# Optimization experiments

Hardware: AMD Instinct MI355X
Metric: run time of the kernel (lower is better)

The kernel has to match this reference:

```python
import jax, jax.numpy as jnp
import numpy as np

N_NODES = 50000
N_EDGES = 800000
IN_DIM = 128
OUT_DIM = 64
NEG_SLOPE = 0.01  # torch F.leaky_relu default


def setup_inputs() -> dict:
    key = jax.random.key(0)
    k1, k2, k3, k4, k5 = jax.random.split(key, 5)
    features = jax.random.normal(k1, (N_NODES, IN_DIM), dtype=jnp.float32)
    # xavier-ish scale for weights
    fc_w = jax.random.normal(k2, (OUT_DIM, IN_DIM), dtype=jnp.float32) * (1.0 / np.sqrt(IN_DIM))
    attn_w = jax.random.normal(k3, (2 * OUT_DIM,), dtype=jnp.float32) * (1.0 / np.sqrt(2 * OUT_DIM))
    src = jax.random.randint(k4, (N_EDGES,), 0, N_NODES, dtype=jnp.int32)
    dst = jax.random.randint(k5, (N_EDGES,), 0, N_NODES, dtype=jnp.int32)
    return {"features": features, "fc_w": fc_w, "attn_w": attn_w, "src": src, "dst": dst}


def reference(features, fc_w, attn_w, src, dst):
    n = features.shape[0]
    out_dim = fc_w.shape[0]
    # z = fc(features), [N, out_dim]
    z = features @ fc_w.T
    # attn_fc([z_src || z_dst]) = z_src @ w_src + z_dst @ w_dst
    a_src = z @ attn_w[:out_dim]   # [N]
    a_dst = z @ attn_w[out_dim:]   # [N]
    e = a_src[src] + a_dst[dst]    # [E] per-edge raw score
    e = jnp.where(e > 0, e, NEG_SLOPE * e)  # leaky_relu
    # edge softmax over incoming edges of each dst node
    e_max = jax.ops.segment_max(e, dst, num_segments=n)      # [N]
    w = jnp.exp(e - e_max[dst])                               # [E]
    denom = jax.ops.segment_sum(w, dst, num_segments=n)       # [N]
    # weighted neighbor sum: sum_e alpha_e * z[src_e]
    num = jax.ops.segment_sum(w[:, None] * z[src], dst, num_segments=n)  # [N, out_dim]
    h = num / jnp.where(denom > 0, denom, 1.0)[:, None]
    # activation = elu
    h = jax.nn.elu(h)
    return h
```

## Files before the change

kernel.cpp:

```cpp
#include <hip/hip_runtime.h>
#include <hip/hip_bf16.h>
#include <hip/hip_fp16.h>

#define N_NODES 50000
#define N_EDGES 800000
#define IN_DIM 128
#define OUT_DIM 64
#define NEG_SLOPE 0.01f
#define NEG_INF (-3.0e38f)

#define N_STRIPS (N_NODES / 16)
#define Z_BLOCKS ((N_STRIPS + 3) / 4)
#define E_I4 (N_EDGES / 4)

#define NB ((N_NODES + 127) / 128)
#define CAP_B 3072
#define CNT_STRIDE 16
#define EB 100
#define CHUNK_I4 (E_I4 / EB)

typedef __bf16 bf16x8 __attribute__((ext_vector_type(8)));
typedef float f32x4 __attribute__((ext_vector_type(4)));

__device__ __forceinline__ unsigned short f2bf_us(float f) {
  __hip_bfloat16 h = __float2bfloat16(f);
  return *reinterpret_cast<unsigned short*>(&h);
}
__device__ __forceinline__ bf16x8 pack_bf16(float4 lo, float4 hi) {
  union { bf16x8 v; unsigned short u[8]; } r;
  r.u[0] = f2bf_us(lo.x); r.u[1] = f2bf_us(lo.y);
  r.u[2] = f2bf_us(lo.z); r.u[3] = f2bf_us(lo.w);
  r.u[4] = f2bf_us(hi.x); r.u[5] = f2bf_us(hi.y);
  r.u[6] = f2bf_us(hi.z); r.u[7] = f2bf_us(hi.w);
  return r.v;
}
__device__ __forceinline__ float bflo(unsigned u) {
  return __uint_as_float(u << 16);
}
__device__ __forceinline__ float bfhi(unsigned u) {
  return __uint_as_float(u & 0xffff0000u);
}

__global__ __launch_bounds__(256) void gat_z_bucket(
    const float* __restrict__ feat, const float* __restrict__ fcw,
    const float* __restrict__ attnw, __hip_bfloat16* __restrict__ z,
    float* __restrict__ asrc, float* __restrict__ adst,
    const int* __restrict__ src, const int* __restrict__ dst,
    int* __restrict__ cnt, unsigned* __restrict__ pairs) {
  if (blockIdx.x >= Z_BLOCKS) {
    __shared__ int hist[NB];
    __shared__ int curs[NB];
    const int tid = threadIdx.x;
    const int i0 = (blockIdx.x - Z_BLOCKS) * CHUNK_I4;
    for (int i = tid; i < NB; i += 256) hist[i] = 0;
    __syncthreads();
    for (int t = i0 + tid; t < i0 + CHUNK_I4; t += 256) {
      int4 d = ((const int4*)dst)[t];
      atomicAdd(&hist[d.x >> 7], 1);
      atomicAdd(&hist[d.y >> 7], 1);
      atomicAdd(&hist[d.z >> 7], 1);
      atomicAdd(&hist[d.w >> 7], 1);
    }
    __syncthreads();
    for (int i = tid; i < NB; i += 256) {
      int h = hist[i];
      curs[i] = h ? atomicAdd(cnt + i * CNT_STRIDE, h) : 0;
    }
    __syncthreads();
    for (int t = i0 + tid; t < i0 + CHUNK_I4; t += 256) {
      int4 s = ((const int4*)src)[t];
      int4 d = ((const int4*)dst)[t];
#define BKT_PUT(dd, ss)                                                    \
  {                                                                        \
    int b = (dd) >> 7;                                                     \
    int r = atomicAdd(&curs[b], 1);                                        \
    if (r < CAP_B)                                                         \
      pairs[(size_t)b * CAP_B + r] =                                       \
          ((unsigned)((dd) & 127) << 16) | (unsigned)(ss);                 \
  }
      BKT_PUT(d.x, s.x)
      BKT_PUT(d.y, s.y)
      BKT_PUT(d.z, s.z)
      BKT_PUT(d.w, s.w)
#undef BKT_PUT
    }
    return;
  }

  const int lane = threadIdx.x & 63;
  const int m = lane & 15;
  const int quad = lane >> 4;
  const int wv = blockIdx.x * 4 + (threadIdx.x >> 6);
  if (wv >= N_STRIPS) return;
  const int n0 = wv * 16;

  bf16x8 bfrag[4][4];
#pragma unroll
  for (int t = 0; t < 4; ++t) {
    const float* wr = fcw + (size_t)(m + 16 * t) * IN_DIM + quad * 8;
#pragma unroll
    for (int c = 0; c < 4; ++c) {
      float4 lo = *(const float4*)(wr + c * 32);
      float4 hi = *(const float4*)(wr + c * 32 + 4);
      bfrag[t][c] = pack_bf16(lo, hi);
    }
  }

  f32x4 acc[4] = {{0.f, 0.f, 0.f, 0.f}, {0.f, 0.f, 0.f, 0.f},
                  {0.f, 0.f, 0.f, 0.f}, {0.f, 0.f, 0.f, 0.f}};
  const float* ar = feat + (size_t)(n0 + m) * IN_DIM + quad * 8;
#pragma unroll
  for (int c = 0; c < 4; ++c) {
    float4 lo = *(const float4*)(ar + c * 32);
    float4 hi = *(const float4*)(ar + c * 32 + 4);
    const bf16x8 af = pack_bf16(lo, hi);
#pragma unroll
    for (int t = 0; t < 4; ++t)
      acc[t] = __builtin_amdgcn_mfma_f32_16x16x32_bf16(af, bfrag[t][c],
                                                       acc[t], 0, 0, 0);
  }

#pragma unroll
  for (int t = 0; t < 4; ++t)
#pragma unroll
    for (int r = 0; r < 4; ++r)
      z[(size_t)(n0 + quad * 4 + r) * OUT_DIM + m + 16 * t] =
          __float2bfloat16(acc[t][r]);

  float aws[4], awd[4];
#pragma unroll
  for (int t = 0; t < 4; ++t) {
    aws[t] = attnw[m + 16 * t];
    awd[t] = attnw[OUT_DIM + m + 16 * t];
  }
  float ps[4], pd[4];
#pragma unroll
  for (int r = 0; r < 4; ++r) {
    float s = 0.f, d = 0.f;
#pragma unroll
    for (int t = 0; t < 4; ++t) {
      s = fmaf(acc[t][r], aws[t], s);
      d = fmaf(acc[t][r], awd[t], d);
    }
    ps[r] = s;
    pd[r] = d;
  }
#pragma unroll
  for (int off = 1; off < 16; off <<= 1) {
#pragma unroll
    for (int r = 0; r < 4; ++r) {
      ps[r] += __shfl_xor(ps[r], off, 64);
      pd[r] += __shfl_xor(pd[r], off, 64);
    }
  }
  if (m == 0) {
#pragma unroll
    for (int r = 0; r < 4; ++r) {
      asrc[n0 + quad * 4 + r] = ps[r];
      adst[n0 + quad * 4 + r] = pd[r];
    }
  }
}

__global__ __launch_bounds__(256) void gat_build_csr(
    const unsigned* __restrict__ pairs, const int* __restrict__ cnt,
    int* __restrict__ offsets, int* __restrict__ ssorted) {
  __shared__ int hist[128], exo[128], cur[128], wsum[4];
  const int b = blockIdx.x;
  const int tid = threadIdx.x;

  int ls = 0;
  for (int i = tid; i < b; i += 256) ls += cnt[i * CNT_STRIDE];
#pragma unroll
  for (int off = 32; off; off >>= 1) ls += __shfl_xor(ls, off, 64);
  if ((tid & 63) == 0) wsum[tid >> 6] = ls;
  if (tid < 128) hist[tid] = 0;
  __syncthreads();
  const int base = wsum[0] + wsum[1] + wsum[2] + wsum[3];

  const int c = min(cnt[b * CNT_STRIDE], CAP_B);
  const unsigned* bp = pairs + (size_t)b * CAP_B;
  for (int i = tid; i < c; i += 256) atomicAdd(&hist[bp[i] >> 16], 1);
  __syncthreads();

  if (tid < 128) exo[tid] = hist[tid];
  __syncthreads();
  for (int off = 1; off < 128; off <<= 1) {
    int u = (tid >= off && tid < 128) ? exo[tid - off] : 0;
    __syncthreads();
    if (tid < 128) exo[tid] += u;
    __syncthreads();
  }
  if (tid < 128) {
    const int ex = exo[tid] - hist[tid];
    cur[tid] = ex;
    const int node = b * 128 + tid;
    if (node < N_NODES) offsets[node] = base + ex;
  }
  if (b == NB - 1 && tid == 0) offsets[N_NODES] = base + c;
  __syncthreads();

  for (int i = tid; i < c; i += 256) {
    const unsigned p = bp[i];
    const int r = atomicAdd(&cur[p >> 16], 1);
    ssorted[base + r] = (int)(p & 0xFFFFu);
  }
}

__global__ __launch_bounds__(256) void gat_agg(
    const __hip_bfloat16* __restrict__ zb, const float* __restrict__ asrc,
    const float* __restrict__ adst, const int* __restrict__ offsets,
    const int* __restrict__ ssorted, float* __restrict__ out) {
  const int lane = threadIdx.x & 63;
  const int j = lane & 7;
  const int eg = lane >> 3;
  const int node = (blockIdx.x * blockDim.x + threadIdx.x) >> 6;
  if (node >= N_NODES) return;
  const uint4* __restrict__ zp4 = (const uint4*)zb;
  const int o0 = offsets[node];
  const int o1 = offsets[node + 1];
  float4* __restrict__ orow = (float4*)(out + (size_t)node * OUT_DIM);
  if (o0 == o1) {
    if (eg == 0) {
      const float4 zv = {0.f, 0.f, 0.f, 0.f};
      orow[2 * j] = zv;
      orow[2 * j + 1] = zv;
    }
    return;
  }
  const float ad = adst[node];

  float m = NEG_INF, dsum = 0.f;
  float acca[8] = {0.f, 0.f, 0.f, 0.f, 0.f, 0.f, 0.f, 0.f};
  float accb[8] = {0.f, 0.f, 0.f, 0.f, 0.f, 0.f, 0.f, 0.f};

  for (int base = o0; base < o1; base += 64) {
    const int cnt = min(64, o1 - base);
    int s = 0;
    float ev = NEG_INF;
    if (lane < cnt) {
      s = ssorted[base + lane];
      float v = asrc[s] + ad;
      ev = v > 0.f ? v : NEG_SLOPE * v;
    }
    float cm = ev;
#pragma unroll
    for (int off = 32; off; off >>= 1) cm = fmaxf(cm, __shfl_xor(cm, off, 64));
    const float nm = fmaxf(m, cm);
    const float scale = __expf(m - nm);
    dsum *= scale;
#pragma unroll
    for (int c = 0; c < 8; ++c) {
      acca[c] *= scale;
      accb[c] *= scale;
    }
    m = nm;

    const float w = (lane < cnt) ? __expf(ev - m) : 0.f;
    dsum += w;
    const unsigned pk =
        (unsigned)s |
        ((unsigned)__half_as_ushort(__float2half(w)) << 16);

    const int ngr = (cnt + 7) >> 3;
    for (int g = 0; g < ngr; g += 2) {
      const unsigned pa = __shfl(pk, 8 * g + eg, 64);
      const int sa = (int)(pa & 0xFFFFu);
      const float wa = __half2float(__ushort_as_half((unsigned short)(pa >> 16)));
      const uint4 ua = zp4[(size_t)sa * 8 + j];
      if (g + 1 < ngr) {
        const unsigned pb = __shfl(pk, 8 * (g + 1) + eg, 64);
        const int sb = (int)(pb & 0xFFFFu);
        const float wb =
            __half2float(__ushort_as_half((unsigned short)(pb >> 16)));
        const uint4 ub = zp4[(size_t)sb * 8 + j];
        accb[0] = fmaf(wb, bflo(ub.x), accb[0]);
        accb[1] = fmaf(wb, bfhi(ub.x), accb[1]);
        accb[2] = fmaf(wb, bflo(ub.y), accb[2]);
        accb[3] = fmaf(wb, bfhi(ub.y), accb[3]);
        accb[4] = fmaf(wb, bflo(ub.z), accb[4]);
        accb[5] = fmaf(wb, bfhi(ub.z), accb[5]);
        accb[6] = fmaf(wb, bflo(ub.w), accb[6]);
        accb[7] = fmaf(wb, bfhi(ub.w), accb[7]);
      }
      acca[0] = fmaf(wa, bflo(ua.x), acca[0]);
      acca[1] = fmaf(wa, bfhi(ua.x), acca[1]);
      acca[2] = fmaf(wa, bflo(ua.y), acca[2]);
      acca[3] = fmaf(wa, bfhi(ua.y), acca[3]);
      acca[4] = fmaf(wa, bflo(ua.z), acca[4]);
      acca[5] = fmaf(wa, bfhi(ua.z), acca[5]);
      acca[6] = fmaf(wa, bflo(ua.w), acca[6]);
      acca[7] = fmaf(wa, bfhi(ua.w), acca[7]);
    }
  }

  float acc[8];
#pragma unroll
  for (int c = 0; c < 8; ++c) acc[c] = acca[c] + accb[c];
#pragma unroll
  for (int off = 8; off < 64; off <<= 1)
#pragma unroll
    for (int c = 0; c < 8; ++c) acc[c] += __shfl_xor(acc[c], off, 64);
#pragma unroll
  for (int off = 32; off; off >>= 1) dsum += __shfl_xor(dsum, off, 64);

  if (eg == 0) {
    const float inv = 1.f / (dsum > 0.f ? dsum : 1.f);
    float4 r0, r1;
    float h;
    h = acc[0] * inv; r0.x = h > 0.f ? h : expm1f(h);
    h = acc[1] * inv; r0.y = h > 0.f ? h : expm1f(h);
    h = acc[2] * inv; r0.z = h > 0.f ? h : expm1f(h);
    h = acc[3] * inv; r0.w = h > 0.f ? h : expm1f(h);
    h = acc[4] * inv; r1.x = h > 0.f ? h : expm1f(h);
    h = acc[5] * inv; r1.y = h > 0.f ? h : expm1f(h);
    h = acc[6] * inv; r1.z = h > 0.f ? h : expm1f(h);
    h = acc[7] * inv; r1.w = h > 0.f ? h : expm1f(h);
    orow[2 * j] = r0;
    orow[2 * j + 1] = r1;
  }
}

extern "C" void kernel_launch(void* const* d_in, const int* in_sizes, int n_in,
                              void* d_out, int out_size, void* d_ws, size_t ws_size,
                              hipStream_t stream) {
  const float* feat  = (const float*)d_in[0];
  const float* fcw   = (const float*)d_in[1];
  const float* attnw = (const float*)d_in[2];
  const int* src     = (const int*)d_in[3];
  const int* dst     = (const int*)d_in[4];
  float* out = (float*)d_out;

  char* ws = (char*)d_ws;
  __hip_bfloat16* z = (__hip_bfloat16*)ws;
  ws += (size_t)N_NODES * OUT_DIM * sizeof(__hip_bfloat16);
  float* asrc = (float*)ws;   ws += (size_t)N_NODES * sizeof(float);
  float* adst = (float*)ws;   ws += (size_t)N_NODES * sizeof(float);
  int* cnt = (int*)ws;        ws += (size_t)NB * CNT_STRIDE * sizeof(int);
  int* offsets = (int*)ws;    ws += (size_t)(N_NODES + 4) * sizeof(int);
  unsigned* pairs = (unsigned*)ws; ws += (size_t)NB * CAP_B * sizeof(unsigned);
  int* ssorted = (int*)ws;    ws += (size_t)N_EDGES * sizeof(int);

  hipMemsetAsync(cnt, 0, (size_t)NB * CNT_STRIDE * sizeof(int), stream);

  gat_z_bucket<<<Z_BLOCKS + EB, 256, 0, stream>>>(
      feat, fcw, attnw, z, asrc, adst, src, dst, cnt, pairs);
  gat_build_csr<<<NB, 256, 0, stream>>>(pairs, cnt, offsets, ssorted);
  gat_agg<<<(N_NODES * 64 + 255) / 256, 256, 0, stream>>>(z, asrc, adst,
                                                          offsets, ssorted, out);
}
```

Measured before the change: 145.3 us.

## Fuse per-bucket CSR build into aggregation kernel using shared-memory sorted sources

Merges the CSR-building and aggregation kernels into one. Each 512-thread block takes half of a 128-node bucket, histograms and scans its 64 nodes in shared memory, scatters source indices into LDS, then runs the online-softmax aggregation with each wave handling 8 nodes. This removes one launch, the global offsets/ssorted writes and their re-reads. In exchange each bucket's pairs are read twice (once per half) and there are fewer, larger blocks with 12KB of LDS each, which can leave load imbalance across waves.

```diff
diff --git a/kernel.cpp b/kernel.cpp
--- a/kernel.cpp
+++ b/kernel.cpp
@@ -162,162 +162,165 @@
   }
 }
 
-__global__ __launch_bounds__(256) void gat_build_csr(
+__global__ __launch_bounds__(512) void gat_csr_agg(
     const unsigned* __restrict__ pairs, const int* __restrict__ cnt,
-    int* __restrict__ offsets, int* __restrict__ ssorted) {
-  __shared__ int hist[128], exo[128], cur[128], wsum[4];
-  const int b = blockIdx.x;
+    const __hip_bfloat16* __restrict__ zb, const float* __restrict__ asrc,
+    const float* __restrict__ adst, float* __restrict__ out) {
+  __shared__ int hist[64];
+  __shared__ int noff[65];
+  __shared__ int cur[64];
+  __shared__ int lsrc[CAP_B];
   const int tid = threadIdx.x;
-
-  int ls = 0;
-  for (int i = tid; i < b; i += 256) ls += cnt[i * CNT_STRIDE];
-#pragma unroll
-  for (int off = 32; off; off >>= 1) ls += __shfl_xor(ls, off, 64);
-  if ((tid & 63) == 0) wsum[tid >> 6] = ls;
-  if (tid < 128) hist[tid] = 0;
+  const int b = blockIdx.x >> 1;
+  const int half = blockIdx.x & 1;
+  const int c = min(cnt[b * CNT_STRIDE], CAP_B);
+  const unsigned* __restrict__ bp = pairs + (size_t)b * CAP_B;
+
+  if (tid < 64) hist[tid] = 0;
   __syncthreads();
-  const int base = wsum[0] + wsum[1] + wsum[2] + wsum[3];
-
-  const int c = min(cnt[b * CNT_STRIDE], CAP_B);
-  const unsigned* bp = pairs + (size_t)b * CAP_B;
-  for (int i = tid; i < c; i += 256) atomicAdd(&hist[bp[i] >> 16], 1);
+  for (int i = tid; i < c; i += 512) {
+    const int ln = (int)(bp[i] >> 16);
+    if ((ln >> 6) == half) atomicAdd(&hist[ln & 63], 1);
+  }
   __syncthreads();
-
-  if (tid < 128) exo[tid] = hist[tid];
+  if (tid < 64) {
+    const int h = hist[tid];
+    int s = h;
+#pragma unroll
+    for (int off = 1; off < 64; off <<= 1) {
+      const int u = __shfl_up(s, off, 64);
+      if (tid >= off) s += u;
+    }
+    noff[tid] = s - h;
+    cur[tid] = s - h;
+    if (tid == 63) noff[64] = s;
+  }
   __syncthreads();
-  for (int off = 1; off < 128; off <<= 1) {
-    int u = (tid >= off && tid < 128) ? exo[tid - off] : 0;
-    __syncthreads();
-    if (tid < 128) exo[tid] += u;
-    __syncthreads();
-  }
-  if (tid < 128) {
-    const int ex = exo[tid] - hist[tid];
-    cur[tid] = ex;
-    const int node = b * 128 + tid;
-    if (node < N_NODES) offsets[node] = base + ex;
-  }
-  if (b == NB - 1 && tid == 0) offsets[N_NODES] = base + c;
+  for (int i = tid; i < c; i += 512) {
+    const unsigned p = bp[i];
+    const int ln = (int)(p >> 16);
+    if ((ln >> 6) == half) {
+      const int r = atomicAdd(&cur[ln & 63], 1);
+      lsrc[r] = (int)(p & 0xFFFFu);
+    }
+  }
   __syncthreads();
 
-  for (int i = tid; i < c; i += 256) {
-    const unsigned p = bp[i];
-    const int r = atomicAdd(&cur[p >> 16], 1);
-    ssorted[base + r] = (int)(p & 0xFFFFu);
-  }
-}
-
-__global__ __launch_bounds__(256) void gat_agg(
-    const __hip_bfloat16* __restrict__ zb, const float* __restrict__ asrc,
-    const float* __restrict__ adst, const int* __restrict__ offsets,
-    const int* __restrict__ ssorted, float* __restrict__ out) {
-  const int lane = threadIdx.x & 63;
+  const int lane = tid & 63;
+  const int wv = tid >> 6;
   const int j = lane & 7;
   const int eg = lane >> 3;
-  const int node = (blockIdx.x * blockDim.x + threadIdx.x) >> 6;
-  if (node >= N_NODES) return;
   const uint4* __restrict__ zp4 = (const uint4*)zb;
-  const int o0 = offsets[node];
-  const int o1 = offsets[node + 1];
-  float4* __restrict__ orow = (float4*)(out + (size_t)node * OUT_DIM);
-  if (o0 == o1) {
+
+#pragma unroll 1
+  for (int k = 0; k < 8; ++k) {
+    const int ln = wv * 8 + k;
+    const int node = b * 128 + half * 64 + ln;
+    if (node >= N_NODES) break;
+    const int o0 = noff[ln];
+    const int o1 = noff[ln + 1];
+    float4* __restrict__ orow = (float4*)(out + (size_t)node * OUT_DIM);
+    if (o0 == o1) {
+      if (eg == 0) {
+        const float4 zv = {0.f, 0.f, 0.f, 0.f};
+        orow[2 * j] = zv;
+        orow[2 * j + 1] = zv;
+      }
+      continue;
+    }
+    const float ad = adst[node];
+
+    float m = NEG_INF, dsum = 0.f;
+    float acca[8] = {0.f, 0.f, 0.f, 0.f, 0.f, 0.f, 0.f, 0.f};
+    float accb[8] = {0.f, 0.f, 0.f, 0.f, 0.f, 0.f, 0.f, 0.f};
+
+    for (int base = o0; base < o1; base += 64) {
+      const int cnt2 = min(64, o1 - base);
+      int s = 0;
+      float ev = NEG_INF;
+      if (lane < cnt2) {
+        s = lsrc[base + lane];
+        const float v = asrc[s] + ad;
+        ev = v > 0.f ? v : NEG_SLOPE * v;
+      }
+      float cm = ev;
+#pragma unroll
+      for (int off = 32; off; off >>= 1)
+        cm = fmaxf(cm, __shfl_xor(cm, off, 64));
+      const float nm = fmaxf(m, cm);
+      const float scale = __expf(m - nm);
+      dsum *= scale;
+#pragma unroll
+      for (int cc = 0; cc < 8; ++cc) {
+        acca[cc] *= scale;
+        accb[cc] *= scale;
+      }
+      m = nm;
+
+      const float w = (lane < cnt2) ? __expf(ev - m) : 0.f;
+      dsum += w;
+      const unsigned pk =
+          (unsigned)s |
+          ((unsigned)__half_as_ushort(__float2half(w)) << 16);
+
+      const int ngr = (cnt2 + 7) >> 3;
+      for (int g = 0; g < ngr; g += 2) {
+        const unsigned pa = __shfl(pk, 8 * g + eg, 64);
+        const int sa = (int)(pa & 0xFFFFu);
+        const float wa =
+            __half2float(__ushort_as_half((unsigned short)(pa >> 16)));
+        const uint4 ua = zp4[(size_t)sa * 8 + j];
+        if (g + 1 < ngr) {
+          const unsigned pb = __shfl(pk, 8 * (g + 1) + eg, 64);
+          const int sb = (int)(pb & 0xFFFFu);
+          const float wb =
+              __half2float(__ushort_as_half((unsigned short)(pb >> 16)));
+          const uint4 ub = zp4[(size_t)sb * 8 + j];
+          accb[0] = fmaf(wb, bflo(ub.x), accb[0]);
+          accb[1] = fmaf(wb, bfhi(ub.x), accb[1]);
+          accb[2] = fmaf(wb, bflo(ub.y), accb[2]);
+          accb[3] = fmaf(wb, bfhi(ub.y), accb[3]);
+          accb[4] = fmaf(wb, bflo(ub.z), accb[4]);
+          accb[5] = fmaf(wb, bfhi(ub.z), accb[5]);
+          accb[6] = fmaf(wb, bflo(ub.w), accb[6]);
+          accb[7] = fmaf(wb, bfhi(ub.w), accb[7]);
+        }
+        acca[0] = fmaf(wa, bflo(ua.x), acca[0]);
+        acca[1] = fmaf(wa, bfhi(ua.x), acca[1]);
+        acca[2] = fmaf(wa, bflo(ua.y), acca[2]);
+        acca[3] = fmaf(wa, bfhi(ua.y), acca[3]);
+        acca[4] = fmaf(wa, bflo(ua.z), acca[4]);
+        acca[5] = fmaf(wa, bfhi(ua.z), acca[5]);
+        acca[6] = fmaf(wa, bflo(ua.w), acca[6]);
+        acca[7] = fmaf(wa, bfhi(ua.w), acca[7]);
+      }
+    }
+
+    float acc[8];
+#pragma unroll
+    for (int cc = 0; cc < 8; ++cc) acc[cc] = acca[cc] + accb[cc];
+#pragma unroll
+    for (int off = 8; off < 64; off <<= 1)
+#pragma unroll
+      for (int cc = 0; cc < 8; ++cc) acc[cc] += __shfl_xor(acc[cc], off, 64);
+#pragma unroll
+    for (int off = 32; off; off >>= 1) dsum += __shfl_xor(dsum, off, 64);
+
     if (eg == 0) {
-      const float4 zv = {0.f, 0.f, 0.f, 0.f};
-      orow[2 * j] = zv;
-      orow[2 * j + 1] = zv;
-    }
-    return;
-  }
-  const float ad = adst[node];
-
-  float m = NEG_INF, dsum = 0.f;
-  float acca[8] = {0.f, 0.f, 0.f, 0.f, 0.f, 0.f, 0.f, 0.f};
-  float accb[8] = {0.f, 0.f, 0.f, 0.f, 0.f, 0.f, 0.f, 0.f};
-
-  for (int base = o0; base < o1; base += 64) {
-    const int cnt = min(64, o1 - base);
-    int s = 0;
-    float ev = NEG_INF;
-    if (lane < cnt) {
-      s = ssorted[base + lane];
-      float v = asrc[s] + ad;
-      ev = v > 0.f ? v : NEG_SLOPE * v;
-    }
-    float cm = ev;
-#pragma unroll
-    for (int off = 32; off; off >>= 1) cm = fmaxf(cm, __shfl_xor(cm, off, 64));
-    const float nm = fmaxf(m, cm);
-    const float scale = __expf(m - nm);
-    dsum *= scale;
-#pragma unroll
-    for (int c = 0; c < 8; ++c) {
-      acca[c] *= scale;
-      accb[c] *= scale;
-    }
-    m = nm;
-
-    const float w = (lane < cnt) ? __expf(ev - m) : 0.f;
-    dsum += w;
-    const unsigned pk =
-        (unsigned)s |
-        ((unsigned)__half_as_ushort(__float2half(w)) << 16);
-
-    const int ngr = (cnt + 7) >> 3;
-    for (int g = 0; g < ngr; g += 2) {
-      const unsigned pa = __shfl(pk, 8 * g + eg, 64);
-      const int sa = (int)(pa & 0xFFFFu);
-      const float wa = __half2float(__ushort_as_half((unsigned short)(pa >> 16)));
-      const uint4 ua = zp4[(size_t)sa * 8 + j];
-      if (g + 1 < ngr) {
-        const unsigned pb = __shfl(pk, 8 * (g + 1) + eg, 64);
-        const int sb = (int)(pb & 0xFFFFu);
-        const float wb =
-            __half2float(__ushort_as_half((unsigned short)(pb >> 16)));
-        const uint4 ub = zp4[(size_t)sb * 8 + j];
-        accb[0] = fmaf(wb, bflo(ub.x), accb[0]);
-        accb[1] = fmaf(wb, bfhi(ub.x), accb[1]);
-        accb[2] = fmaf(wb, bflo(ub.y), accb[2]);
-        accb[3] = fmaf(wb, bfhi(ub.y), accb[3]);
-        accb[4] = fmaf(wb, bflo(ub.z), accb[4]);
-        accb[5] = fmaf(wb, bfhi(ub.z), accb[5]);
-        accb[6] = fmaf(wb, bflo(ub.w), accb[6]);
-        accb[7] = fmaf(wb, bfhi(ub.w), accb[7]);
-      }
-      acca[0] = fmaf(wa, bflo(ua.x), acca[0]);
-      acca[1] = fmaf(wa, bfhi(ua.x), acca[1]);
-      acca[2] = fmaf(wa, bflo(ua.y), acca[2]);
-      acca[3] = fmaf(wa, bfhi(ua.y), acca[3]);
-      acca[4] = fmaf(wa, bflo(ua.z), acca[4]);
-      acca[5] = fmaf(wa, bfhi(ua.z), acca[5]);
-      acca[6] = fmaf(wa, bflo(ua.w), acca[6]);
-      acca[7] = fmaf(wa, bfhi(ua.w), acca[7]);
-    }
-  }
-
-  float acc[8];
-#pragma unroll
-  for (int c = 0; c < 8; ++c) acc[c] = acca[c] + accb[c];
-#pragma unroll
-  for (int off = 8; off < 64; off <<= 1)
-#pragma unroll
-    for (int c = 0; c < 8; ++c) acc[c] += __shfl_xor(acc[c], off, 64);
-#pragma unroll
-  for (int off = 32; off; off >>= 1) dsum += __shfl_xor(dsum, off, 64);
-
-  if (eg == 0) {
-    const float inv = 1.f / (dsum > 0.f ? dsum : 1.f);
-    float4 r0, r1;
-    float h;
-    h = acc[0] * inv; r0.x = h > 0.f ? h : expm1f(h);
-    h = acc[1] * inv; r0.y = h > 0.f ? h : expm1f(h);
-    h = acc[2] * inv; r0.z = h > 0.f ? h : expm1f(h);
-    h = acc[3] * inv; r0.w = h > 0.f ? h : expm1f(h);
-    h = acc[4] * inv; r1.x = h > 0.f ? h : expm1f(h);
-    h = acc[5] * inv; r1.y = h > 0.f ? h : expm1f(h);
-    h = acc[6] * inv; r1.z = h > 0.f ? h : expm1f(h);
-    h = acc[7] * inv; r1.w = h > 0.f ? h : expm1f(h);
-    orow[2 * j] = r0;
-    orow[2 * j + 1] = r1;
+      const float inv = 1.f / (dsum > 0.f ? dsum : 1.f);
+      float4 r0, r1;
+      float h;
+      h = acc[0] * inv; r0.x = h > 0.f ? h : expm1f(h);
+      h = acc[1] * inv; r0.y = h > 0.f ? h : expm1f(h);
+      h = acc[2] * inv; r0.z = h > 0.f ? h : expm1f(h);
+      h = acc[3] * inv; r0.w = h > 0.f ? h : expm1f(h);
+      h = acc[4] * inv; r1.x = h > 0.f ? h : expm1f(h);
+      h = acc[5] * inv; r1.y = h > 0.f ? h : expm1f(h);
+      h = acc[6] * inv; r1.z = h > 0.f ? h : expm1f(h);
+      h = acc[7] * inv; r1.w = h > 0.f ? h : expm1f(h);
+      orow[2 * j] = r0;
+      orow[2 * j + 1] = r1;
+    }
   }
 }
 
@@ -337,15 +340,11 @@
   float* asrc = (float*)ws;   ws += (size_t)N_NODES * sizeof(float);
   float* adst = (float*)ws;   ws += (size_t)N_NODES * sizeof(float);
   int* cnt = (int*)ws;        ws += (size_t)NB * CNT_STRIDE * sizeof(int);
-  int* offsets = (int*)ws;    ws += (size_t)(N_NODES + 4) * sizeof(int);
   unsigned* pairs = (unsigned*)ws; ws += (size_t)NB * CAP_B * sizeof(unsigned);
-  int* ssorted = (int*)ws;    ws += (size_t)N_EDGES * sizeof(int);
 
   hipMemsetAsync(cnt, 0, (size_t)NB * CNT_STRIDE * sizeof(int), stream);
 
   gat_z_bucket<<<Z_BLOCKS + EB, 256, 0, stream>>>(
       feat, fcw, attnw, z, asrc, adst, src, dst, cnt, pairs);
-  gat_build_csr<<<NB, 256, 0, stream>>>(pairs, cnt, offsets, ssorted);
-  gat_agg<<<(N_NODES * 64 + 255) / 256, 256, 0, stream>>>(z, asrc, adst,
-                                                          offsets, ssorted, out);
-}
+  gat_csr_agg<<<NB * 2, 512, 0, stream>>>(pairs, cnt, z, asrc, adst, out);
+}
```

Result: slower. 149.3 us (+2.8%).
